# Optimization experiments

Hardware: AMD Instinct MI355X
Metric: run time of the kernel (lower is better)

Reference implementation:

```python
import jax, jax.numpy as jnp
import numpy as np

EPS = 1e-15
SCALING = 2.0  # softmax scaling in AttentionReference.forward default


def _psd(xs, mask):
    """ESPnet get_power_spectral_density_matrix with fused einsum.
    xs:   (B, F, C, T) complex64
    mask: (B, F, C, T) float32
    returns psd: (B, F, C, C) complex64
    """
    m = mask.mean(axis=-2)                               # (B, F, T)
    m = m / (m.sum(axis=-1, keepdims=True) + EPS)        # normalize over T
    # fused masked covariance: sum_t m[t] * x[:,t] x[:,t]^H
    return jnp.einsum('bfct,bft,bfet->bfce', xs, m.astype(xs.dtype), jnp.conj(xs))


def _attention_reference(psd_in, mlp_w, mlp_b, gvec_w, gvec_b):
    """AttentionReference.forward. psd_in: (B,F,C,C) complex -> u: (B,C)."""
    C = psd_in.shape[-1]
    eye = jnp.eye(C, dtype=bool)
    psd = jnp.where(eye, jnp.zeros((), psd_in.dtype), psd_in)   # zero diagonal
    psd = jnp.swapaxes(psd.sum(axis=-1) / (C - 1), -1, -2)      # (B, C, F)
    psd_feat = jnp.sqrt(psd.real ** 2 + psd.imag ** 2)          # (B, C, F)
    mlp = jnp.tanh(psd_feat @ mlp_w + mlp_b)                    # (B, C, A)
    e = (mlp @ gvec_w + gvec_b)[..., 0]                         # (B, C)
    return jax.nn.softmax(SCALING * e, axis=-1)                 # (B, C)


def _mvdr_vector(psd_s, psd_n, u):
    """get_mvdr_vector: ws = inv(psd_n) @ psd_s / trace(.) then contract with u."""
    numerator = jnp.linalg.inv(psd_n) @ psd_s                   # (B, F, C, C)
    trace = jnp.einsum('bfcc->bf', numerator)
    ws_mat = numerator / (trace[..., None, None] + EPS)
    return jnp.einsum('bfec,bc->bfe', ws_mat, u.astype(ws_mat.dtype))  # (B, F, C)


def setup_inputs() -> dict:
    key = jax.random.key(0)
    ks = jax.random.split(key, 6)
    B, T, C, F, A = 8, 512, 8, 257, 320
    return {
        'data_real': jax.random.normal(ks[0], (B, T, C, F), jnp.float32),
        'data_imag': jax.random.normal(ks[1], (B, T, C, F), jnp.float32),
        'mask_speech': jax.random.uniform(ks[2], (B, F, C, T), jnp.float32),
        'mask_noise': jax.random.uniform(ks[3], (B, F, C, T), jnp.float32),
        'mlp_w': jax.random.normal(ks[4], (F, A), jnp.float32) / np.sqrt(F),
        'mlp_b': jnp.zeros((A,), jnp.float32),
        'gvec_w': jax.random.normal(ks[5], (A, 1), jnp.float32) / np.sqrt(A),
        'gvec_b': jnp.zeros((1,), jnp.float32),
        'ilens': jnp.full((B,), T, dtype=jnp.int32),
    }


def reference(data_real, data_imag, mask_speech, mask_noise,
              mlp_w, mlp_b, gvec_w, gvec_b, ilens):
    # data: (B,T,C,F) -> permute(0,3,2,1) -> (B,F,C,T)
    data = jnp.transpose(data_real + 1j * data_imag, (0, 3, 2, 1)).astype(jnp.complex64)
    psd_speech = _psd(data, mask_speech)    # (B,F,C,C)
    psd_noise = _psd(data, mask_noise)      # (B,F,C,C)
    u = _attention_reference(psd_speech, mlp_w, mlp_b, gvec_w, gvec_b)  # (B,C)
    ws = _mvdr_vector(psd_speech, psd_noise, u)                         # (B,F,C)
    # apply_beamforming_vector: conj(ws) . data over channels -> (B,F,T)
    enhanced = jnp.einsum('bfc,bfct->bft', jnp.conj(ws), data)
    enhanced = jnp.swapaxes(enhanced, -1, -2)                           # (B,T,F)
    # complex output packed as real (B,T,F,2)
    return jnp.stack([enhanced.real, enhanced.imag], axis=-1)
```

## Files before the change

### kernel.cpp

```cpp
#include <hip/hip_runtime.h>
#include <math.h>

#define TTOT 512
#define CCH 8
#define FFR 257
#define AAH 320
#define NBF 2056
#define BF2 2112
#define NTIL 16
#define EPSF 1e-15f
#define WSB (FFR * 8)

#define OFF_MBAR 0
#define SZ_MBAR (2 * 512 * BF2)
#define OFF_PART (OFF_MBAR + SZ_MBAR)
#define SZ_PART (144 * NTIL * BF2)
#define OFF_PSDS (OFF_PART + SZ_PART)
#define SZ_PSD (NBF * 128)
#define OFF_PSDN (OFF_PSDS + SZ_PSD)
#define OFF_E (OFF_PSDN + SZ_PSD)
#define OFF_WS (OFF_E + 64)

__device__ __constant__ int c_pi[36] = {0,0,0,0,0,0,0,0, 1,1,1,1,1,1,1, 2,2,2,2,2,2,
                                        3,3,3,3,3, 4,4,4,4, 5,5,5, 6,6, 7};
__device__ __constant__ int c_pj[36] = {0,1,2,3,4,5,6,7, 1,2,3,4,5,6,7, 2,3,4,5,6,7,
                                        3,4,5,6,7, 4,5,6,7, 5,6,7, 6,7, 7};

__global__ __launch_bounds__(256) void k_mask(
    const float* __restrict__ mask_s, const float* __restrict__ mask_n,
    float* __restrict__ mbar) {
  int bf = blockIdx.x;
  int tid = threadIdx.x;
  int lane = tid & 63, wv = tid >> 6;
  const float2* ms = (const float2*)(mask_s + (size_t)bf * CCH * TTOT);
  const float2* mn = (const float2*)(mask_n + (size_t)bf * CCH * TTOT);
  float2 ss = make_float2(0.f, 0.f), sn = make_float2(0.f, 0.f);
#pragma unroll
  for (int c = 0; c < 8; ++c) {
    float2 a = ms[c * 256 + tid];
    ss.x += a.x; ss.y += a.y;
    float2 b = mn[c * 256 + tid];
    sn.x += b.x; sn.y += b.y;
  }
  float tots = ss.x + ss.y, totn = sn.x + sn.y;
#pragma unroll
  for (int off = 32; off > 0; off >>= 1) {
    tots += __shfl_down(tots, off);
    totn += __shfl_down(totn, off);
  }
  __shared__ float reds[4], redn[4];
  if (lane == 0) { reds[wv] = tots; redn[wv] = totn; }
  __syncthreads();
  float totS = reds[0] + reds[1] + reds[2] + reds[3];
  float totN = redn[0] + redn[1] + redn[2] + redn[3];
  float invs = 1.f / (totS * 0.125f + EPSF);
  float invn = 1.f / (totN * 0.125f + EPSF);
  int t0 = 2 * tid;
  mbar[(size_t)t0 * BF2 + bf] = ss.x * 0.125f * invs;
  mbar[(size_t)(t0 + 1) * BF2 + bf] = ss.y * 0.125f * invs;
  mbar[(size_t)(512 + t0) * BF2 + bf] = sn.x * 0.125f * invn;
  mbar[(size_t)(512 + t0 + 1) * BF2 + bf] = sn.y * 0.125f * invn;
}

__global__ __launch_bounds__(256) void k_psd(
    const float* __restrict__ dr, const float* __restrict__ di,
    const float* __restrict__ mbar, float* __restrict__ partial) {
  int lane = threadIdx.x & 63, wv = threadIdx.x >> 6;
  int bfb = blockIdx.x;
  int ttile = blockIdx.y;
  int bf = bfb * 64 + lane;
  if (bf > NBF - 1) bf = NBF - 1;
  int b = bf / FFR, f = bf - b * FFR;
  size_t dbase = (size_t)b * TTOT * CCH * FFR + f;
  int t0 = ttile * 32 + wv * 8;

  float acc[36][4];
#pragma unroll
  for (int p = 0; p < 36; ++p) {
    acc[p][0] = 0.f; acc[p][1] = 0.f; acc[p][2] = 0.f; acc[p][3] = 0.f;
  }

  for (int tt = 0; tt < 8; ++tt) {
    int t = t0 + tt;
    const float* pr = dr + dbase + (size_t)t * (CCH * FFR);
    const float* pi = di + dbase + (size_t)t * (CCH * FFR);
    float xre[8], xim[8];
#pragma unroll
    for (int c = 0; c < 8; ++c) { xre[c] = pr[c * FFR]; xim[c] = pi[c * FFR]; }
    float m_s = mbar[(size_t)t * BF2 + bf];
    float m_n = mbar[(size_t)(512 + t) * BF2 + bf];
    int p = 0;
#pragma unroll
    for (int i = 0; i < 8; ++i)
#pragma unroll
      for (int j = i; j < 8; ++j) {
        float pre = xre[i] * xre[j] + xim[i] * xim[j];
        float pim = xim[i] * xre[j] - xre[i] * xim[j];
        acc[p][0] += m_s * pre; acc[p][1] += m_s * pim;
        acc[p][2] += m_n * pre; acc[p][3] += m_n * pim;
        ++p;
      }
  }

  __shared__ float scr[4][36][65];
#pragma unroll
  for (int r = 0; r < 4; ++r) {
    if (r) __syncthreads();
#pragma unroll
    for (int pp = 0; pp < 9; ++pp)
#pragma unroll
      for (int mc = 0; mc < 4; ++mc)
        scr[wv][pp * 4 + mc][lane] = acc[r * 9 + pp][mc];
    __syncthreads();
#pragma unroll
    for (int k = 0; k < 9; ++k) {
      int v = wv * 9 + k;
      float s = scr[0][v][lane] + scr[1][v][lane] + scr[2][v][lane] + scr[3][v][lane];
      int g = r * 36 + v;
      partial[((size_t)g * NTIL + ttile) * BF2 + bfb * 64 + lane] = s;
    }
  }
}

__global__ __launch_bounds__(256) void k_reduce(
    const float* __restrict__ partial, float* __restrict__ psd_s,
    float* __restrict__ psd_n) {
  int lane = threadIdx.x & 63, wv = threadIdx.x >> 6;
  int bf = blockIdx.x * 64 + lane;
  float vals[9][4];
#pragma unroll
  for (int pp = 0; pp < 9; ++pp)
#pragma unroll
    for (int mc = 0; mc < 4; ++mc) {
      int g = (wv * 9 + pp) * 4 + mc;
      const float* src = partial + (size_t)g * NTIL * BF2 + blockIdx.x * 64 + lane;
      float s = 0.f;
#pragma unroll
      for (int nt = 0; nt < NTIL; ++nt) s += src[nt * BF2];
      vals[pp][mc] = s;
    }
  if (bf < NBF) {
    size_t base = (size_t)bf * 128;
#pragma unroll
    for (int pp = 0; pp < 9; ++pp) {
      int p = wv * 9 + pp;
      int i = c_pi[p], j = c_pj[p];
      float sre = vals[pp][0], sim = vals[pp][1];
      float nre = vals[pp][2], nim = vals[pp][3];
      psd_s[base + (i * 8 + j) * 2] = sre;
      psd_s[base + (i * 8 + j) * 2 + 1] = sim;
      psd_s[base + (j * 8 + i) * 2] = sre;
      psd_s[base + (j * 8 + i) * 2 + 1] = -sim;
      psd_n[base + (i * 8 + j) * 2] = nre;
      psd_n[base + (i * 8 + j) * 2 + 1] = nim;
      psd_n[base + (j * 8 + i) * 2] = nre;
      psd_n[base + (j * 8 + i) * 2 + 1] = -nim;
    }
  }
}

__global__ __launch_bounds__(320) void k2_attn(
    const float* __restrict__ psd_s, const float* __restrict__ mlp_w,
    const float* __restrict__ mlp_b, const float* __restrict__ gvec_w,
    float* __restrict__ e_out) {
  __shared__ float feat[FFR];
  __shared__ float wred[5];
  int bx = blockIdx.x;
  int b = bx >> 3, c = bx & 7;
  int tid = threadIdx.x;
  int lane = tid & 63, wv = tid >> 6;
  if (tid < FFR) {
    const float* p = psd_s + (((size_t)(b * FFR + tid)) * 8 + c) * 16;
    float sre = 0.f, sim = 0.f;
#pragma unroll
    for (int e = 0; e < 8; ++e) {
      if (e != c) { sre += p[e * 2]; sim += p[e * 2 + 1]; }
    }
    sre *= (1.0f / 7.0f);
    sim *= (1.0f / 7.0f);
    feat[tid] = sqrtf(sre * sre + sim * sim);
  }
  __syncthreads();
  float acc = mlp_b[tid];
  for (int f = 0; f < FFR; ++f) acc += feat[f] * mlp_w[f * AAH + tid];
  float v = tanhf(acc) * gvec_w[tid];
#pragma unroll
  for (int off = 32; off > 0; off >>= 1) v += __shfl_down(v, off);
  if (lane == 0) wred[wv] = v;
  __syncthreads();
  if (tid == 0) e_out[bx] = wred[0] + wred[1] + wred[2] + wred[3] + wred[4];
}

__global__ __launch_bounds__(256) void k3_mvdr(
    const float* __restrict__ psd_s, const float* __restrict__ psd_n,
    const float* __restrict__ e_in, const float* __restrict__ gvec_b,
    float* __restrict__ ws) {
  int lane = threadIdx.x & 63, wv = threadIdx.x >> 6;
  int bf = blockIdx.x * 4 + wv;
  int b = bf / FFR;
  int r = lane >> 3, c = lane & 7;
  float2 n = ((const float2*)(psd_n + (size_t)bf * 128))[lane];
  float2 s = ((const float2*)(psd_s + (size_t)bf * 128))[lane];

#pragma unroll
  for (int k = 0; k < 8; ++k) {
    float pvre = __shfl(n.x, k * 9), pvim = __shfl(n.y, k * 9);
    float dinv = 1.f / (pvre * pvre + pvim * pvim);
    float pire = pvre * dinv, piim = -pvim * dinv;
    if (r == k) {
      float2 nn = n, ss = s;
      n.x = nn.x * pire - nn.y * piim; n.y = nn.x * piim + nn.y * pire;
      s.x = ss.x * pire - ss.y * piim; s.y = ss.x * piim + ss.y * pire;
    }
    float fre = __shfl(n.x, r * 8 + k), fim = __shfl(n.y, r * 8 + k);
    float pnre = __shfl(n.x, k * 8 + c), pnim = __shfl(n.y, k * 8 + c);
    float psre = __shfl(s.x, k * 8 + c), psim = __shfl(s.y, k * 8 + c);
    if (r != k) {
      n.x -= fre * pnre - fim * pnim; n.y -= fre * pnim + fim * pnre;
      s.x -= fre * psre - fim * psim; s.y -= fre * psim + fim * psre;
    }
  }
  float trx = (r == c) ? s.x : 0.f, tryy = (r == c) ? s.y : 0.f;
#pragma unroll
  for (int off = 1; off < 64; off <<= 1) {
    trx += __shfl_xor(trx, off);
    tryy += __shfl_xor(tryy, off);
  }
  float val = 2.f * (e_in[b * 8 + c] + gvec_b[0]);
  float mx = val;
#pragma unroll
  for (int off = 1; off < 8; off <<= 1) mx = fmaxf(mx, __shfl_xor(mx, off));
  float pe = expf(val - mx);
  float psum = pe;
#pragma unroll
  for (int off = 1; off < 8; off <<= 1) psum += __shfl_xor(psum, off);
  float uc = pe / psum;
  float wre = s.x * uc, wim = s.y * uc;
#pragma unroll
  for (int off = 1; off < 8; off <<= 1) {
    wre += __shfl_xor(wre, off);
    wim += __shfl_xor(wim, off);
  }
  float tre = trx + EPSF, tim = tryy;
  float d2 = 1.f / (tre * tre + tim * tim);
  float owre = (wre * tre + wim * tim) * d2;
  float owim = (wim * tre - wre * tim) * d2;
  if (c == 0) ((float2*)ws)[(size_t)bf * 8 + r] = make_float2(owre, owim);
}

__global__ __launch_bounds__(256) void k4_beam(
    const float* __restrict__ dr, const float* __restrict__ di,
    const float* __restrict__ ws, float* __restrict__ out) {
  __shared__ float2 wsp[FFR * 9];
  int b = blockIdx.y;
  int t0 = blockIdx.x * 4;
  int tid = threadIdx.x;
  const float2* wsg = (const float2*)ws + (size_t)b * WSB;
  for (int i = tid; i < FFR * 8; i += 256) {
    int f = i >> 3, c = i & 7;
    wsp[f * 9 + c] = wsg[i];
  }
  __syncthreads();
  for (int ts = 0; ts < 4; ++ts) {
    int t = t0 + ts;
    const float* drb = dr + (size_t)(b * TTOT + t) * (CCH * FFR);
    const float* dib = di + (size_t)(b * TTOT + t) * (CCH * FFR);
    for (int f = tid; f < FFR; f += 256) {
      float are = 0.f, aim = 0.f;
#pragma unroll
      for (int c = 0; c < 8; ++c) {
        float xre = drb[c * FFR + f];
        float xim = dib[c * FFR + f];
        float2 w = wsp[f * 9 + c];
        are += w.x * xre + w.y * xim;
        aim += w.x * xim - w.y * xre;
      }
      ((float2*)out)[(size_t)(b * TTOT + t) * FFR + f] = make_float2(are, aim);
    }
  }
}

extern "C" void kernel_launch(void* const* d_in, const int* in_sizes, int n_in,
                              void* d_out, int out_size, void* d_ws, size_t ws_size,
                              hipStream_t stream) {
  const float* dr = (const float*)d_in[0];
  const float* di = (const float*)d_in[1];
  const float* mask_s = (const float*)d_in[2];
  const float* mask_n = (const float*)d_in[3];
  const float* mlp_w = (const float*)d_in[4];
  const float* mlp_b = (const float*)d_in[5];
  const float* gvec_w = (const float*)d_in[6];
  const float* gvec_b = (const float*)d_in[7];
  float* out = (float*)d_out;

  float* wsf = (float*)d_ws;
  float* mbar = wsf + OFF_MBAR;
  float* part = wsf + OFF_PART;
  float* psd_s = wsf + OFF_PSDS;
  float* psd_n = wsf + OFF_PSDN;
  float* e_arr = wsf + OFF_E;
  float* wsv = wsf + OFF_WS;

  hipLaunchKernelGGL(k_mask, dim3(NBF), dim3(256), 0, stream, mask_s, mask_n, mbar);
  hipLaunchKernelGGL(k_psd, dim3(33, NTIL), dim3(256), 0, stream, dr, di, mbar, part);
  hipLaunchKernelGGL(k_reduce, dim3(33), dim3(256), 0, stream, part, psd_s, psd_n);
  hipLaunchKernelGGL(k2_attn, dim3(64), dim3(320), 0, stream,
                     psd_s, mlp_w, mlp_b, gvec_w, e_arr);
  hipLaunchKernelGGL(k3_mvdr, dim3(514), dim3(256), 0, stream,
                     psd_s, psd_n, e_arr, gvec_b, wsv);
  hipLaunchKernelGGL(k4_beam, dim3(128, 8), dim3(256), 0, stream, dr, di, wsv, out);
}
```

Baseline: 270.0 us.

## Split PSD channel pairs into per-wave quadrants and drop LDS cross-wave reduction

k_psd previously gave each wave a slice of timesteps covering all 36 upper-triangular channel pairs, then merged the waves through shared memory. Now each wave owns one 4x4 quadrant of the 8x8 covariance and loops over all 32 timesteps, so the shared-memory reduction and its barriers go away. The cost is computing the full matrix (64 pairs instead of 36), redundant data loads across waves, and a larger partial buffer. The mask-mean buffers are switched to bf-major layout so k_mask writes are coalesced, at the price of strided per-lane reads in k_psd. The reduce kernel is spread over a 2D grid with one output element per thread, and the attention MLP loop gets an unroll pragma.

```diff
diff --git a/kernel.cpp b/kernel.cpp
--- a/kernel.cpp
+++ b/kernel.cpp
@@ -8,27 +8,21 @@
 #define NBF 2056
 #define BF2 2112
 #define NTIL 16
+#define TTILE 32
 #define EPSF 1e-15f
 #define WSB (FFR * 8)
 
-#define OFF_MBAR 0
-#define SZ_MBAR (2 * 512 * BF2)
-#define OFF_PART (OFF_MBAR + SZ_MBAR)
-#define SZ_PART (144 * NTIL * BF2)
-#define OFF_PSDS (OFF_PART + SZ_PART)
-#define SZ_PSD (NBF * 128)
-#define OFF_PSDN (OFF_PSDS + SZ_PSD)
-#define OFF_E (OFF_PSDN + SZ_PSD)
+#define OFF_MBS 0
+#define OFF_MBN (OFF_MBS + NBF * 512)
+#define OFF_PART (OFF_MBN + NBF * 512)
+#define OFF_PSDS (OFF_PART + NTIL * 256 * BF2)
+#define OFF_PSDN (OFF_PSDS + NBF * 128)
+#define OFF_E (OFF_PSDN + NBF * 128)
 #define OFF_WS (OFF_E + 64)
-
-__device__ __constant__ int c_pi[36] = {0,0,0,0,0,0,0,0, 1,1,1,1,1,1,1, 2,2,2,2,2,2,
-                                        3,3,3,3,3, 4,4,4,4, 5,5,5, 6,6, 7};
-__device__ __constant__ int c_pj[36] = {0,1,2,3,4,5,6,7, 1,2,3,4,5,6,7, 2,3,4,5,6,7,
-                                        3,4,5,6,7, 4,5,6,7, 5,6,7, 6,7, 7};
 
 __global__ __launch_bounds__(256) void k_mask(
     const float* __restrict__ mask_s, const float* __restrict__ mask_n,
-    float* __restrict__ mbar) {
+    float* __restrict__ mbar_s, float* __restrict__ mbar_n) {
   int bf = blockIdx.x;
   int tid = threadIdx.x;
   int lane = tid & 63, wv = tid >> 6;
@@ -53,18 +47,16 @@
   __syncthreads();
   float totS = reds[0] + reds[1] + reds[2] + reds[3];
   float totN = redn[0] + redn[1] + redn[2] + redn[3];
-  float invs = 1.f / (totS * 0.125f + EPSF);
-  float invn = 1.f / (totN * 0.125f + EPSF);
-  int t0 = 2 * tid;
-  mbar[(size_t)t0 * BF2 + bf] = ss.x * 0.125f * invs;
-  mbar[(size_t)(t0 + 1) * BF2 + bf] = ss.y * 0.125f * invs;
-  mbar[(size_t)(512 + t0) * BF2 + bf] = sn.x * 0.125f * invn;
-  mbar[(size_t)(512 + t0 + 1) * BF2 + bf] = sn.y * 0.125f * invn;
+  float invs = 0.125f / (totS * 0.125f + EPSF);
+  float invn = 0.125f / (totN * 0.125f + EPSF);
+  ((float2*)(mbar_s + (size_t)bf * TTOT))[tid] = make_float2(ss.x * invs, ss.y * invs);
+  ((float2*)(mbar_n + (size_t)bf * TTOT))[tid] = make_float2(sn.x * invn, sn.y * invn);
 }
 
 __global__ __launch_bounds__(256) void k_psd(
     const float* __restrict__ dr, const float* __restrict__ di,
-    const float* __restrict__ mbar, float* __restrict__ partial) {
+    const float* __restrict__ mbar_s, const float* __restrict__ mbar_n,
+    float* __restrict__ partial) {
   int lane = threadIdx.x & 63, wv = threadIdx.x >> 6;
   int bfb = blockIdx.x;
   int ttile = blockIdx.y;
@@ -72,90 +64,76 @@
   if (bf > NBF - 1) bf = NBF - 1;
   int b = bf / FFR, f = bf - b * FFR;
   size_t dbase = (size_t)b * TTOT * CCH * FFR + f;
-  int t0 = ttile * 32 + wv * 8;
-
-  float acc[36][4];
-#pragma unroll
-  for (int p = 0; p < 36; ++p) {
+  int qi = (wv >> 1) * 4, qj = (wv & 1) * 4;
+  bool diag = (qi == qj);
+  int t0 = ttile * TTILE;
+
+  float acc[16][4];
+#pragma unroll
+  for (int p = 0; p < 16; ++p) {
     acc[p][0] = 0.f; acc[p][1] = 0.f; acc[p][2] = 0.f; acc[p][3] = 0.f;
   }
 
-  for (int tt = 0; tt < 8; ++tt) {
+#pragma unroll 2
+  for (int tt = 0; tt < TTILE; ++tt) {
     int t = t0 + tt;
     const float* pr = dr + dbase + (size_t)t * (CCH * FFR);
-    const float* pi = di + dbase + (size_t)t * (CCH * FFR);
-    float xre[8], xim[8];
-#pragma unroll
-    for (int c = 0; c < 8; ++c) { xre[c] = pr[c * FFR]; xim[c] = pi[c * FFR]; }
-    float m_s = mbar[(size_t)t * BF2 + bf];
-    float m_n = mbar[(size_t)(512 + t) * BF2 + bf];
-    int p = 0;
-#pragma unroll
-    for (int i = 0; i < 8; ++i)
-#pragma unroll
-      for (int j = i; j < 8; ++j) {
-        float pre = xre[i] * xre[j] + xim[i] * xim[j];
-        float pim = xim[i] * xre[j] - xre[i] * xim[j];
-        acc[p][0] += m_s * pre; acc[p][1] += m_s * pim;
-        acc[p][2] += m_n * pre; acc[p][3] += m_n * pim;
-        ++p;
+    const float* pim_ = di + dbase + (size_t)t * (CCH * FFR);
+    float ir[4], ii[4], jr[4], ji[4];
+#pragma unroll
+    for (int k = 0; k < 4; ++k) {
+      ir[k] = pr[(qi + k) * FFR];
+      ii[k] = pim_[(qi + k) * FFR];
+    }
+    if (!diag) {
+#pragma unroll
+      for (int k = 0; k < 4; ++k) {
+        jr[k] = pr[(qj + k) * FFR];
+        ji[k] = pim_[(qj + k) * FFR];
       }
-  }
-
-  __shared__ float scr[4][36][65];
-#pragma unroll
-  for (int r = 0; r < 4; ++r) {
-    if (r) __syncthreads();
-#pragma unroll
-    for (int pp = 0; pp < 9; ++pp)
-#pragma unroll
-      for (int mc = 0; mc < 4; ++mc)
-        scr[wv][pp * 4 + mc][lane] = acc[r * 9 + pp][mc];
-    __syncthreads();
-#pragma unroll
-    for (int k = 0; k < 9; ++k) {
-      int v = wv * 9 + k;
-      float s = scr[0][v][lane] + scr[1][v][lane] + scr[2][v][lane] + scr[3][v][lane];
-      int g = r * 36 + v;
-      partial[((size_t)g * NTIL + ttile) * BF2 + bfb * 64 + lane] = s;
-    }
-  }
+    } else {
+#pragma unroll
+      for (int k = 0; k < 4; ++k) { jr[k] = ir[k]; ji[k] = ii[k]; }
+    }
+    float m_s = mbar_s[(size_t)bf * TTOT + t];
+    float m_n = mbar_n[(size_t)bf * TTOT + t];
+#pragma unroll
+    for (int i4 = 0; i4 < 4; ++i4)
+#pragma unroll
+      for (int j4 = 0; j4 < 4; ++j4) {
+        int p = i4 * 4 + j4;
+        float pre = ir[i4] * jr[j4] + ii[i4] * ji[j4];
+        float pimv = ii[i4] * jr[j4] - ir[i4] * ji[j4];
+        acc[p][0] += m_s * pre; acc[p][1] += m_s * pimv;
+        acc[p][2] += m_n * pre; acc[p][3] += m_n * pimv;
+      }
+  }
+
+  size_t pbase = (size_t)ttile * 256 * BF2 + (size_t)wv * 64 * BF2 + bfb * 64 + lane;
+#pragma unroll
+  for (int p = 0; p < 16; ++p)
+#pragma unroll
+    for (int comp = 0; comp < 4; ++comp)
+      partial[pbase + (size_t)(p * 4 + comp) * BF2] = acc[p][comp];
 }
 
 __global__ __launch_bounds__(256) void k_reduce(
     const float* __restrict__ partial, float* __restrict__ psd_s,
     float* __restrict__ psd_n) {
   int lane = threadIdx.x & 63, wv = threadIdx.x >> 6;
-  int bf = blockIdx.x * 64 + lane;
-  float vals[9][4];
-#pragma unroll
-  for (int pp = 0; pp < 9; ++pp)
-#pragma unroll
-    for (int mc = 0; mc < 4; ++mc) {
-      int g = (wv * 9 + pp) * 4 + mc;
-      const float* src = partial + (size_t)g * NTIL * BF2 + blockIdx.x * 64 + lane;
-      float s = 0.f;
-#pragma unroll
-      for (int nt = 0; nt < NTIL; ++nt) s += src[nt * BF2];
-      vals[pp][mc] = s;
-    }
+  int bfb = blockIdx.x;
+  int g = blockIdx.y * 4 + wv;
+  int bf = bfb * 64 + lane;
+  const float* src = partial + (size_t)g * BF2 + bfb * 64 + lane;
+  float s = 0.f;
+#pragma unroll
+  for (int nt = 0; nt < NTIL; ++nt) s += src[(size_t)nt * 256 * BF2];
   if (bf < NBF) {
-    size_t base = (size_t)bf * 128;
-#pragma unroll
-    for (int pp = 0; pp < 9; ++pp) {
-      int p = wv * 9 + pp;
-      int i = c_pi[p], j = c_pj[p];
-      float sre = vals[pp][0], sim = vals[pp][1];
-      float nre = vals[pp][2], nim = vals[pp][3];
-      psd_s[base + (i * 8 + j) * 2] = sre;
-      psd_s[base + (i * 8 + j) * 2 + 1] = sim;
-      psd_s[base + (j * 8 + i) * 2] = sre;
-      psd_s[base + (j * 8 + i) * 2 + 1] = -sim;
-      psd_n[base + (i * 8 + j) * 2] = nre;
-      psd_n[base + (i * 8 + j) * 2 + 1] = nim;
-      psd_n[base + (j * 8 + i) * 2] = nre;
-      psd_n[base + (j * 8 + i) * 2 + 1] = -nim;
-    }
+    int w = g >> 6, rem = g & 63, p = rem >> 2, comp = rem & 3;
+    int i = (w >> 1) * 4 + (p >> 2);
+    int j = (w & 1) * 4 + (p & 3);
+    float* dst = (comp < 2) ? psd_s : psd_n;
+    dst[(size_t)bf * 128 + (i * 8 + j) * 2 + (comp & 1)] = s;
   }
 }
 
@@ -182,6 +160,7 @@
   }
   __syncthreads();
   float acc = mlp_b[tid];
+#pragma unroll 8
   for (int f = 0; f < FFR; ++f) acc += feat[f] * mlp_w[f * AAH + tid];
   float v = tanhf(acc) * gvec_w[tid];
 #pragma unroll
@@ -294,16 +273,20 @@
   float* out = (float*)d_out;
 
   float* wsf = (float*)d_ws;
-  float* mbar = wsf + OFF_MBAR;
+  float* mbar_s = wsf + OFF_MBS;
+  float* mbar_n = wsf + OFF_MBN;
   float* part = wsf + OFF_PART;
   float* psd_s = wsf + OFF_PSDS;
   float* psd_n = wsf + OFF_PSDN;
   float* e_arr = wsf + OFF_E;
   float* wsv = wsf + OFF_WS;
 
-  hipLaunchKernelGGL(k_mask, dim3(NBF), dim3(256), 0, stream, mask_s, mask_n, mbar);
-  hipLaunchKernelGGL(k_psd, dim3(33, NTIL), dim3(256), 0, stream, dr, di, mbar, part);
-  hipLaunchKernelGGL(k_reduce, dim3(33), dim3(256), 0, stream, part, psd_s, psd_n);
+  hipLaunchKernelGGL(k_mask, dim3(NBF), dim3(256), 0, stream,
+                     mask_s, mask_n, mbar_s, mbar_n);
+  hipLaunchKernelGGL(k_psd, dim3(33, NTIL), dim3(256), 0, stream,
+                     dr, di, mbar_s, mbar_n, part);
+  hipLaunchKernelGGL(k_reduce, dim3(33, 64), dim3(256), 0, stream,
+                     part, psd_s, psd_n);
   hipLaunchKernelGGL(k2_attn, dim3(64), dim3(320), 0, stream,
                      psd_s, mlp_w, mlp_b, gvec_w, e_arr);
   hipLaunchKernelGGL(k3_mvdr, dim3(514), dim3(256), 0, stream,
```

Measured after the change: 296.6 us. 1.1x slower.
